# Kernel optimization log

Hardware: AMD Instinct MI355X
Metric: run time of the kernel (lower is better)

## Reference

```python
import jax, jax.numpy as jnp
import numpy as np


def setup_inputs() -> dict:
    key = jax.random.key(0)
    k1, k2 = jax.random.split(key)
    B, Tc, Tq, D = 8, 2048, 1024, 1024
    similarity = jax.random.normal(k1, (B, Tc, Tq), dtype=jnp.float32)
    qencode = jax.random.normal(k2, (B, Tq, D), dtype=jnp.float32)
    return {"similarity": similarity, "qencode": qencode}


def reference(similarity, qencode):
    # softmax over query axis, then weighted sum of query encodings:
    # equivalent to softmax(similarity, -1) @ qencode, avoiding the
    # [B, Tc, Tq, D] broadcasted intermediate of the original TF code.
    attn = jax.nn.softmax(similarity, axis=-1)          # [B, Tc, Tq]
    c2q = jnp.einsum("bcq,bqd->bcd", attn, qencode)     # [B, Tc, D]
    return c2q
```

## Files before the change

kernel.cpp:

```cpp
#include <hip/hip_runtime.h>
#include <hip/hip_bf16.h>
#include <stdint.h>

#define BATCH 8
#define TC 2048
#define TQ 1024
#define DD 1024

typedef __attribute__((ext_vector_type(8))) __bf16 bf16x8;
typedef __attribute__((ext_vector_type(4))) float f32x4;

__device__ __forceinline__ ushort f2bf(float f) {
    uint32_t u = __float_as_uint(f);
    uint32_t r = (u + 0x7fffu + ((u >> 16) & 1u)) >> 16;
    return (ushort)r;
}

__global__ __launch_bounds__(256) void prep(const float* __restrict__ sim,
                                            const float* __restrict__ qen,
                                            ushort* __restrict__ attn,
                                            ushort* __restrict__ qt) {
    __shared__ float tile[64][65];
    const int t = threadIdx.x;
    if (blockIdx.x < 4096) {
        const int wid = t >> 6;
        const int lane = t & 63;
        const int row = blockIdx.x * 4 + wid;
        const float4* src = (const float4*)(sim + (size_t)row * TQ);

        float4 x[4];
        #pragma unroll
        for (int j = 0; j < 4; j++) x[j] = src[lane + 64 * j];

        float m = -INFINITY;
        #pragma unroll
        for (int j = 0; j < 4; j++)
            m = fmaxf(m, fmaxf(fmaxf(x[j].x, x[j].y), fmaxf(x[j].z, x[j].w)));
        #pragma unroll
        for (int o = 32; o >= 1; o >>= 1) m = fmaxf(m, __shfl_xor(m, o));

        const float L2E = 1.4426950408889634f;
        float e[4][4];
        float s = 0.f;
        #pragma unroll
        for (int j = 0; j < 4; j++) {
            e[j][0] = exp2f((x[j].x - m) * L2E);
            e[j][1] = exp2f((x[j].y - m) * L2E);
            e[j][2] = exp2f((x[j].z - m) * L2E);
            e[j][3] = exp2f((x[j].w - m) * L2E);
            s += (e[j][0] + e[j][1]) + (e[j][2] + e[j][3]);
        }
        #pragma unroll
        for (int o = 32; o >= 1; o >>= 1) s += __shfl_xor(s, o);
        const float inv = 1.0f / s;

        ushort4* dst = (ushort4*)(attn + (size_t)row * TQ);
        #pragma unroll
        for (int j = 0; j < 4; j++) {
            ushort4 o4;
            o4.x = f2bf(e[j][0] * inv);
            o4.y = f2bf(e[j][1] * inv);
            o4.z = f2bf(e[j][2] * inv);
            o4.w = f2bf(e[j][3] * inv);
            dst[lane + 64 * j] = o4;
        }
    } else {
        const int bid = blockIdx.x - 4096;
        const int b = bid >> 8;
        const int rem = bid & 255;
        const int q0 = (rem >> 4) * 64;
        const int d0 = (rem & 15) * 64;
        const int r = t >> 4;
        const int c = (t & 15) * 4;

        #pragma unroll
        for (int it = 0; it < 4; it++) {
            float4 v = *(const float4*)(qen + ((size_t)b * TQ + q0 + r + it * 16) * DD + d0 + c);
            tile[r + it * 16][c + 0] = v.x;
            tile[r + it * 16][c + 1] = v.y;
            tile[r + it * 16][c + 2] = v.z;
            tile[r + it * 16][c + 3] = v.w;
        }
        __syncthreads();

        #pragma unroll
        for (int it = 0; it < 4; it++) {
            const int d = (t >> 4) + it * 16;
            const int qq = (t & 15) * 4;
            ushort4 o4;
            o4.x = f2bf(tile[qq + 0][d]);
            o4.y = f2bf(tile[qq + 1][d]);
            o4.z = f2bf(tile[qq + 2][d]);
            o4.w = f2bf(tile[qq + 3][d]);
            *(ushort4*)(qt + ((size_t)b * DD + d0 + d) * TQ + q0 + qq) = o4;
        }
    }
}

__global__ __launch_bounds__(256, 2) void gemm_bf16(const ushort* __restrict__ A,
                                                    const ushort* __restrict__ Bt,
                                                    float* __restrict__ C) {
    __shared__ __align__(16) ushort As[128 * 64];
    __shared__ __align__(16) ushort Bs[128 * 64];

    const int flat = blockIdx.x;
    const int b = flat >> 7;
    const int rem = flat & 127;
    const int group = rem >> 5;
    const int mi_t = group * 4 + (rem & 3);
    const int ni_t = (rem >> 2) & 7;
    const int tm0 = mi_t * 128;
    const int tn0 = ni_t * 128;

    const ushort* Ab = A + (size_t)b * TC * TQ;
    const ushort* Bb = Bt + (size_t)b * DD * TQ;
    float* Cb = C + (size_t)b * TC * DD;

    const int t = threadIdx.x;
    const int w = t >> 6, lane = t & 63;
    const int quad = lane >> 4, l16 = lane & 15;
    const int wm = (w >> 1) * 64, wn = (w & 1) * 64;

    f32x4 acc[4][4];
    #pragma unroll
    for (int i = 0; i < 4; i++)
        #pragma unroll
        for (int j = 0; j < 4; j++) acc[i][j] = (f32x4){0.f, 0.f, 0.f, 0.f};

    const int srow = w * 8 + (lane >> 3);
    const int sk = ((lane & 7) ^ (lane >> 3)) * 8;

    const int rkey = l16 & 7;

    for (int kk = 0; kk < TQ; kk += 64) {
        #pragma unroll
        for (int i = 0; i < 4; i++) {
            const ushort* ga = Ab + (size_t)(tm0 + i * 32 + srow) * TQ + kk + sk;
            const ushort* gb = Bb + (size_t)(tn0 + i * 32 + srow) * TQ + kk + sk;
            char* la = (char*)As + i * 4096 + w * 1024;
            char* lb = (char*)Bs + i * 4096 + w * 1024;
            __builtin_amdgcn_global_load_lds(
                (const __attribute__((address_space(1))) void*)ga,
                (__attribute__((address_space(3))) void*)la, 16, 0, 0);
            __builtin_amdgcn_global_load_lds(
                (const __attribute__((address_space(1))) void*)gb,
                (__attribute__((address_space(3))) void*)lb, 16, 0, 0);
        }
        __syncthreads();

        #pragma unroll
        for (int s = 0; s < 2; s++) {
            const int rswz = ((s * 4 + quad) ^ rkey) * 8;
            bf16x8 af[4], bfr[4];
            #pragma unroll
            for (int mi = 0; mi < 4; mi++)
                af[mi] = *(const bf16x8*)&As[(wm + mi * 16 + l16) * 64 + rswz];
            #pragma unroll
            for (int ni = 0; ni < 4; ni++)
                bfr[ni] = *(const bf16x8*)&Bs[(wn + ni * 16 + l16) * 64 + rswz];

            #pragma unroll
            for (int mi = 0; mi < 4; mi++)
                #pragma unroll
                for (int ni = 0; ni < 4; ni++)
                    acc[mi][ni] = __builtin_amdgcn_mfma_f32_16x16x32_bf16(
                        af[mi], bfr[ni], acc[mi][ni], 0, 0, 0);
        }
        __syncthreads();
    }

    #pragma unroll
    for (int mi = 0; mi < 4; mi++) {
        const int r0 = tm0 + wm + mi * 16 + quad * 4;
        #pragma unroll
        for (int ni = 0; ni < 4; ni++) {
            const int c = tn0 + wn + ni * 16 + l16;
            f32x4 v = acc[mi][ni];
            #pragma unroll
            for (int r = 0; r < 4; r++) Cb[(size_t)(r0 + r) * DD + c] = v[r];
        }
    }
}

extern "C" void kernel_launch(void* const* d_in, const int* in_sizes, int n_in,
                              void* d_out, int out_size, void* d_ws, size_t ws_size,
                              hipStream_t stream) {
    const float* sim = (const float*)d_in[0];
    const float* qen = (const float*)d_in[1];
    float* out = (float*)d_out;

    ushort* attn = (ushort*)d_ws;
    ushort* qt = (ushort*)d_ws + (size_t)BATCH * TC * TQ;

    prep<<<4096 + 2048, 256, 0, stream>>>(sim, qen, attn, qt);
    gemm_bf16<<<BATCH * (TC / 128) * (DD / 128), 256, 0, stream>>>(attn, qt, out);
}
```

Before: 178.2 us.

## Rewrite GEMM as 256x256 tile, 8-wave, double-buffered pipelined kernel

Replaces the 128x128 single-buffered GEMM with a 256x256 tile and 512 threads. LDS is double-buffered and global->LDS loads are interleaved with MFMA sub-phases using barriers, waitcnt and setprio to overlap memory with compute. A new block swizzle maps tiles to blocks. The larger tile raises arithmetic intensity but leaves only 256 blocks, which may underfill the GPU, and it uses 128KB of LDS and many accumulator registers.

```diff
diff --git a/kernel.cpp b/kernel.cpp
--- a/kernel.cpp
+++ b/kernel.cpp
@@ -97,87 +97,161 @@
     }
 }
 
-__global__ __launch_bounds__(256, 2) void gemm_bf16(const ushort* __restrict__ A,
+#define BAR()   __builtin_amdgcn_s_barrier()
+#define LGKM0() asm volatile("s_waitcnt lgkmcnt(0)" ::: "memory")
+#define PRIO(x) __builtin_amdgcn_s_setprio(x)
+
+#define KTILE(BUF, S1, S2, S3, S4, WEND)                                           \
+    {                                                                              \
+        bf16x8 aLO[4][2], aHI[4][2], bLO[2][2], bHI[2][2];                         \
+                         \
+        _Pragma("unroll") for (int mi = 0; mi < 4; ++mi)                           \
+            _Pragma("unroll") for (int ss = 0; ss < 2; ++ss)                       \
+                aLO[mi][ss] = *(const bf16x8*)&As[BUF][wm][mi * 16 + l16]          \
+                                  [((ss * 4 + quad) ^ rkey) * 8];                  \
+        _Pragma("unroll") for (int ni = 0; ni < 2; ++ni)                           \
+            _Pragma("unroll") for (int ss = 0; ss < 2; ++ss)                       \
+                bLO[ni][ss] = *(const bf16x8*)&Bs[BUF][wbh][wrow + ni * 16 + l16]  \
+                                  [((ss * 4 + quad) ^ rkey) * 8];                  \
+        S1;                                                                        \
+        BAR(); LGKM0(); PRIO(1);                                                   \
+        _Pragma("unroll") for (int mi = 0; mi < 4; ++mi)                           \
+            _Pragma("unroll") for (int ni = 0; ni < 2; ++ni)                       \
+                _Pragma("unroll") for (int ss = 0; ss < 2; ++ss)                   \
+                    acc[mi][ni] = __builtin_amdgcn_mfma_f32_16x16x32_bf16(         \
+                        aLO[mi][ss], bLO[ni][ss], acc[mi][ni], 0, 0, 0);           \
+        PRIO(0); BAR();                                                            \
+                                             \
+        _Pragma("unroll") for (int mi = 0; mi < 4; ++mi)                           \
+            _Pragma("unroll") for (int ss = 0; ss < 2; ++ss)                       \
+                aHI[mi][ss] = *(const bf16x8*)&As[BUF][wm][64 + mi * 16 + l16]     \
+                                  [((ss * 4 + quad) ^ rkey) * 8];                  \
+        S2;                                                                        \
+        BAR(); LGKM0(); PRIO(1);                                                   \
+        _Pragma("unroll") for (int mi = 0; mi < 4; ++mi)                           \
+            _Pragma("unroll") for (int ni = 0; ni < 2; ++ni)                       \
+                _Pragma("unroll") for (int ss = 0; ss < 2; ++ss)                   \
+                    acc[4 + mi][ni] = __builtin_amdgcn_mfma_f32_16x16x32_bf16(     \
+                        aHI[mi][ss], bLO[ni][ss], acc[4 + mi][ni], 0, 0, 0);       \
+        PRIO(0); BAR();                                                            \
+                                                    \
+        _Pragma("unroll") for (int ni = 0; ni < 2; ++ni)                           \
+            _Pragma("unroll") for (int ss = 0; ss < 2; ++ss)                       \
+                bHI[ni][ss] = *(const bf16x8*)&Bs[BUF][wbh]                        \
+                                  [wrow + 32 + ni * 16 + l16]                      \
+                                  [((ss * 4 + quad) ^ rkey) * 8];                  \
+        S3;                                                                        \
+        BAR(); LGKM0(); PRIO(1);                                                   \
+        _Pragma("unroll") for (int mi = 0; mi < 4; ++mi)                           \
+            _Pragma("unroll") for (int ni = 0; ni < 2; ++ni)                       \
+                _Pragma("unroll") for (int ss = 0; ss < 2; ++ss)                   \
+                    acc[mi][2 + ni] = __builtin_amdgcn_mfma_f32_16x16x32_bf16(     \
+                        aLO[mi][ss], bHI[ni][ss], acc[mi][2 + ni], 0, 0, 0);       \
+        PRIO(0); BAR();                                                            \
+                                                  \
+        S4;                                                                        \
+        BAR(); PRIO(1);                                                            \
+        _Pragma("unroll") for (int mi = 0; mi < 4; ++mi)                           \
+            _Pragma("unroll") for (int ni = 0; ni < 2; ++ni)                       \
+                _Pragma("unroll") for (int ss = 0; ss < 2; ++ss)                   \
+                    acc[4 + mi][2 + ni] = __builtin_amdgcn_mfma_f32_16x16x32_bf16( \
+                        aHI[mi][ss], bHI[ni][ss], acc[4 + mi][2 + ni], 0, 0, 0);   \
+        PRIO(0);                                                                   \
+        WEND;                                                                      \
+        BAR();                                                                     \
+    }
+
+__global__ __launch_bounds__(512, 2) void gemm_bf16(const ushort* __restrict__ A,
                                                     const ushort* __restrict__ Bt,
                                                     float* __restrict__ C) {
-    __shared__ __align__(16) ushort As[128 * 64];
-    __shared__ __align__(16) ushort Bs[128 * 64];
-
-    const int flat = blockIdx.x;
-    const int b = flat >> 7;
-    const int rem = flat & 127;
-    const int group = rem >> 5;
-    const int mi_t = group * 4 + (rem & 3);
-    const int ni_t = (rem >> 2) & 7;
-    const int tm0 = mi_t * 128;
-    const int tn0 = ni_t * 128;
+    __shared__ __align__(16) ushort As[2][2][128][64];
+    __shared__ __align__(16) ushort Bs[2][2][128][64];
+
+    const int bid = blockIdx.x;
+    const int swz = ((bid & 7) << 5) | (bid >> 3);
+    const int b   = swz >> 5;
+    const int tm0 = ((swz >> 2) & 7) * 256;
+    const int tn0 = (swz & 3) * 256;
 
     const ushort* Ab = A + (size_t)b * TC * TQ;
     const ushort* Bb = Bt + (size_t)b * DD * TQ;
     float* Cb = C + (size_t)b * TC * DD;
 
     const int t = threadIdx.x;
-    const int w = t >> 6, lane = t & 63;
+    const int wid = t >> 6, lane = t & 63;
     const int quad = lane >> 4, l16 = lane & 15;
-    const int wm = (w >> 1) * 64, wn = (w & 1) * 64;
-
-    f32x4 acc[4][4];
+    const int wm = wid >> 2;
+    const int wn = wid & 3;
+    const int wbh = wn >> 1;
+    const int wrow = (wn & 1) << 6;
+    const int rkey = l16 & 7;
+
+    const int srow = t >> 3;
+    const int gko  = (((t & 7) ^ (srow & 7)) << 3);
+
+    auto stageA = [&](int buf, int h, int kk) {
+        const ushort* g0 = Ab + (size_t)(tm0 + h * 128 + srow) * TQ + kk + gko;
+        char* l0 = (char*)(&As[buf][h][0][0]) + wid * 1024;
+        __builtin_amdgcn_global_load_lds(
+            (const __attribute__((address_space(1))) void*)g0,
+            (__attribute__((address_space(3))) void*)l0, 16, 0, 0);
+        __builtin_amdgcn_global_load_lds(
+            (const __attribute__((address_space(1))) void*)(g0 + (size_t)64 * TQ),
+            (__attribute__((address_space(3))) void*)(l0 + 8192), 16, 0, 0);
+    };
+    auto stageB = [&](int buf, int h, int kk) {
+        const ushort* g0 = Bb + (size_t)(tn0 + h * 128 + srow) * TQ + kk + gko;
+        char* l0 = (char*)(&Bs[buf][h][0][0]) + wid * 1024;
+        __builtin_amdgcn_global_load_lds(
+            (const __attribute__((address_space(1))) void*)g0,
+            (__attribute__((address_space(3))) void*)l0, 16, 0, 0);
+        __builtin_amdgcn_global_load_lds(
+            (const __attribute__((address_space(1))) void*)(g0 + (size_t)64 * TQ),
+            (__attribute__((address_space(3))) void*)(l0 + 8192), 16, 0, 0);
+    };
+
+    f32x4 acc[8][4];
     #pragma unroll
-    for (int i = 0; i < 4; i++)
+    for (int i = 0; i < 8; i++)
         #pragma unroll
         for (int j = 0; j < 4; j++) acc[i][j] = (f32x4){0.f, 0.f, 0.f, 0.f};
 
-    const int srow = w * 8 + (lane >> 3);
-    const int sk = ((lane & 7) ^ (lane >> 3)) * 8;
-
-    const int rkey = l16 & 7;
-
-    for (int kk = 0; kk < TQ; kk += 64) {
-        #pragma unroll
-        for (int i = 0; i < 4; i++) {
-            const ushort* ga = Ab + (size_t)(tm0 + i * 32 + srow) * TQ + kk + sk;
-            const ushort* gb = Bb + (size_t)(tn0 + i * 32 + srow) * TQ + kk + sk;
-            char* la = (char*)As + i * 4096 + w * 1024;
-            char* lb = (char*)Bs + i * 4096 + w * 1024;
-            __builtin_amdgcn_global_load_lds(
-                (const __attribute__((address_space(1))) void*)ga,
-                (__attribute__((address_space(3))) void*)la, 16, 0, 0);
-            __builtin_amdgcn_global_load_lds(
-                (const __attribute__((address_space(1))) void*)gb,
-                (__attribute__((address_space(3))) void*)lb, 16, 0, 0);
-        }
-        __syncthreads();
-
-        #pragma unroll
-        for (int s = 0; s < 2; s++) {
-            const int rswz = ((s * 4 + quad) ^ rkey) * 8;
-            bf16x8 af[4], bfr[4];
-            #pragma unroll
-            for (int mi = 0; mi < 4; mi++)
-                af[mi] = *(const bf16x8*)&As[(wm + mi * 16 + l16) * 64 + rswz];
-            #pragma unroll
-            for (int ni = 0; ni < 4; ni++)
-                bfr[ni] = *(const bf16x8*)&Bs[(wn + ni * 16 + l16) * 64 + rswz];
-
-            #pragma unroll
-            for (int mi = 0; mi < 4; mi++)
-                #pragma unroll
-                for (int ni = 0; ni < 4; ni++)
-                    acc[mi][ni] = __builtin_amdgcn_mfma_f32_16x16x32_bf16(
-                        af[mi], bfr[ni], acc[mi][ni], 0, 0, 0);
-        }
-        __syncthreads();
-    }
+    stageA(0, 0, 0);  stageA(0, 1, 0);  stageB(0, 0, 0);  stageB(0, 1, 0);
+    stageA(1, 0, 64); stageA(1, 1, 64); stageB(1, 0, 64); stageB(1, 1, 64);
+    asm volatile("s_waitcnt vmcnt(8)" ::: "memory");
+    BAR();
+
+    #pragma unroll 1
+    for (int it = 0; it < 7; ++it) {
+        const int kA = (2 * it + 2) * 64;
+        const int kB = (2 * it + 3) * 64;
+        KTILE(0,
+              (void)0,
+              (void)0,
+              stageA(0, 0, kA),
+              stageA(0, 1, kA),
+              asm volatile("s_waitcnt vmcnt(4)" ::: "memory"));
+        KTILE(1,
+              stageB(0, 0, kA),
+              stageB(0, 1, kA),
+              (stageA(1, 0, kB), stageA(1, 1, kB)),
+              (stageB(1, 0, kB), stageB(1, 1, kB)),
+              asm volatile("s_waitcnt vmcnt(8)" ::: "memory"));
+    }
+
+    KTILE(0, (void)0, (void)0, (void)0, (void)0,
+          asm volatile("s_waitcnt vmcnt(0)" ::: "memory"));
+    KTILE(1, (void)0, (void)0, (void)0, (void)0, (void)0);
 
     #pragma unroll
-    for (int mi = 0; mi < 4; mi++) {
-        const int r0 = tm0 + wm + mi * 16 + quad * 4;
-        #pragma unroll
-        for (int ni = 0; ni < 4; ni++) {
-            const int c = tn0 + wn + ni * 16 + l16;
+    for (int mi = 0; mi < 8; ++mi) {
+        const int r0 = tm0 + wm * 128 + mi * 16 + quad * 4;
+        #pragma unroll
+        for (int ni = 0; ni < 4; ++ni) {
+            const int c = tn0 + wn * 64 + ni * 16 + l16;
             f32x4 v = acc[mi][ni];
             #pragma unroll
-            for (int r = 0; r < 4; r++) Cb[(size_t)(r0 + r) * DD + c] = v[r];
+            for (int r = 0; r < 4; ++r) Cb[(size_t)(r0 + r) * DD + c] = v[r];
         }
     }
 }
@@ -193,5 +267,5 @@
     ushort* qt = (ushort*)d_ws + (size_t)BATCH * TC * TQ;
 
     prep<<<4096 + 2048, 256, 0, stream>>>(sim, qen, attn, qt);
-    gemm_bf16<<<BATCH * (TC / 128) * (DD / 128), 256, 0, stream>>>(attn, qt, out);
-}
+    gemm_bf16<<<BATCH * (TC / 256) * (DD / 256), 512, 0, stream>>>(attn, qt, out);
+}
```

After: 180.0 us. No clear change (+1.1%).

## Rewrite GEMM as 256x256 tile, 8-wave double-buffered pipeline with interleaved MFMA

Applied to the files above, without the earlier changes.

The bf16 GEMM now uses 256x256 output tiles with 512 threads per block and a double-buffered LDS ring. The next K-slice is prefetched with global_load_lds while the current one is consumed. LDS fragment reads are interleaved with MFMA groups under explicit lgkmcnt waits and s_setprio, and the block index is swizzled across batches. The goal is to hide global-load latency and raise arithmetic intensity per tile. In exchange it uses more LDS and registers (128 KB LDS per block and a larger accumulator array), and with 256 blocks on a GPU with many CUs occupancy may be limited.

```diff
diff --git a/kernel.cpp b/kernel.cpp
--- a/kernel.cpp
+++ b/kernel.cpp
@@ -97,87 +97,193 @@
     }
 }
 
-__global__ __launch_bounds__(256, 2) void gemm_bf16(const ushort* __restrict__ A,
+#define BAR()    __builtin_amdgcn_s_barrier()
+#define LGKM(n)  asm volatile("s_waitcnt lgkmcnt(" #n ")" ::: "memory")
+#define VMCNT0() asm volatile("s_waitcnt vmcnt(0)" ::: "memory")
+#define PRIO(x)  __builtin_amdgcn_s_setprio(x)
+
+__global__ __launch_bounds__(512, 2) void gemm_bf16(const ushort* __restrict__ A,
                                                     const ushort* __restrict__ Bt,
                                                     float* __restrict__ C) {
-    __shared__ __align__(16) ushort As[128 * 64];
-    __shared__ __align__(16) ushort Bs[128 * 64];
-
-    const int flat = blockIdx.x;
-    const int b = flat >> 7;
-    const int rem = flat & 127;
-    const int group = rem >> 5;
-    const int mi_t = group * 4 + (rem & 3);
-    const int ni_t = (rem >> 2) & 7;
-    const int tm0 = mi_t * 128;
-    const int tn0 = ni_t * 128;
+    __shared__ __align__(16) ushort As[2][2][128][64];
+    __shared__ __align__(16) ushort Bs[2][2][128][64];
+
+    const int bid = blockIdx.x;
+    const int swz = ((bid & 7) << 5) | (bid >> 3);
+    const int b   = swz >> 5;
+    const int tm0 = ((swz >> 2) & 7) * 256;
+    const int tn0 = (swz & 3) * 256;
 
     const ushort* Ab = A + (size_t)b * TC * TQ;
     const ushort* Bb = Bt + (size_t)b * DD * TQ;
     float* Cb = C + (size_t)b * TC * DD;
 
     const int t = threadIdx.x;
-    const int w = t >> 6, lane = t & 63;
+    const int wid = t >> 6, lane = t & 63;
     const int quad = lane >> 4, l16 = lane & 15;
-    const int wm = (w >> 1) * 64, wn = (w & 1) * 64;
-
-    f32x4 acc[4][4];
+    const int wm = wid >> 2;
+    const int wn = wid & 3;
+    const int wbh = wn >> 1;
+    const int wrow = (wn & 1) << 6;
+    const int rkey = l16 & 7;
+
+    const int srow = t >> 3;
+    const int gko  = (((t & 7) ^ (srow & 7)) << 3);
+
+    auto stageA = [&](int buf, int h, int kk) {
+        const ushort* g0 = Ab + (size_t)(tm0 + h * 128 + srow) * TQ + kk + gko;
+        char* l0 = (char*)(&As[buf][h][0][0]) + wid * 1024;
+        __builtin_amdgcn_global_load_lds(
+            (const __attribute__((address_space(1))) void*)g0,
+            (__attribute__((address_space(3))) void*)l0, 16, 0, 0);
+        __builtin_amdgcn_global_load_lds(
+            (const __attribute__((address_space(1))) void*)(g0 + (size_t)64 * TQ),
+            (__attribute__((address_space(3))) void*)(l0 + 8192), 16, 0, 0);
+    };
+    auto stageB = [&](int buf, int h, int kk) {
+        const ushort* g0 = Bb + (size_t)(tn0 + h * 128 + srow) * TQ + kk + gko;
+        char* l0 = (char*)(&Bs[buf][h][0][0]) + wid * 1024;
+        __builtin_amdgcn_global_load_lds(
+            (const __attribute__((address_space(1))) void*)g0,
+            (__attribute__((address_space(3))) void*)l0, 16, 0, 0);
+        __builtin_amdgcn_global_load_lds(
+            (const __attribute__((address_space(1))) void*)(g0 + (size_t)64 * TQ),
+            (__attribute__((address_space(3))) void*)(l0 + 8192), 16, 0, 0);
+    };
+
+    auto rdA = [&](int buf, int rb, int ss) -> bf16x8 {
+        return *(const bf16x8*)&As[buf][wm][rb * 16 + l16][((ss * 4 + quad) ^ rkey) * 8];
+    };
+    auto rdB = [&](int buf, int nb, int ss) -> bf16x8 {
+        return *(const bf16x8*)&Bs[buf][wbh][wrow + nb * 16 + l16][((ss * 4 + quad) ^ rkey) * 8];
+    };
+
+    f32x4 acc[8][4];
     #pragma unroll
-    for (int i = 0; i < 4; i++)
+    for (int i = 0; i < 8; i++)
         #pragma unroll
         for (int j = 0; j < 4; j++) acc[i][j] = (f32x4){0.f, 0.f, 0.f, 0.f};
 
-    const int srow = w * 8 + (lane >> 3);
-    const int sk = ((lane & 7) ^ (lane >> 3)) * 8;
-
-    const int rkey = l16 & 7;
-
-    for (int kk = 0; kk < TQ; kk += 64) {
-        #pragma unroll
-        for (int i = 0; i < 4; i++) {
-            const ushort* ga = Ab + (size_t)(tm0 + i * 32 + srow) * TQ + kk + sk;
-            const ushort* gb = Bb + (size_t)(tn0 + i * 32 + srow) * TQ + kk + sk;
-            char* la = (char*)As + i * 4096 + w * 1024;
-            char* lb = (char*)Bs + i * 4096 + w * 1024;
-            __builtin_amdgcn_global_load_lds(
-                (const __attribute__((address_space(1))) void*)ga,
-                (__attribute__((address_space(3))) void*)la, 16, 0, 0);
-            __builtin_amdgcn_global_load_lds(
-                (const __attribute__((address_space(1))) void*)gb,
-                (__attribute__((address_space(3))) void*)lb, 16, 0, 0);
-        }
-        __syncthreads();
-
-        #pragma unroll
-        for (int s = 0; s < 2; s++) {
-            const int rswz = ((s * 4 + quad) ^ rkey) * 8;
-            bf16x8 af[4], bfr[4];
-            #pragma unroll
-            for (int mi = 0; mi < 4; mi++)
-                af[mi] = *(const bf16x8*)&As[(wm + mi * 16 + l16) * 64 + rswz];
-            #pragma unroll
-            for (int ni = 0; ni < 4; ni++)
-                bfr[ni] = *(const bf16x8*)&Bs[(wn + ni * 16 + l16) * 64 + rswz];
-
-            #pragma unroll
-            for (int mi = 0; mi < 4; mi++)
-                #pragma unroll
-                for (int ni = 0; ni < 4; ni++)
-                    acc[mi][ni] = __builtin_amdgcn_mfma_f32_16x16x32_bf16(
-                        af[mi], bfr[ni], acc[mi][ni], 0, 0, 0);
-        }
-        __syncthreads();
+    stageA(0, 0, 0); stageA(0, 1, 0); stageB(0, 0, 0); stageB(0, 1, 0);
+    VMCNT0();
+
+    #pragma unroll 1
+    for (int x = 0; x < 16; ++x) {
+        const int bs = x & 1;
+        BAR();
+
+        bf16x8 aS0[4], aS1[4], bS0[2], bS1[2], c0[2], c1[2], d0[4], d1[4], e0[2], e1[2];
+
+        #pragma unroll
+        for (int i = 0; i < 4; i++) aS0[i] = rdA(bs, i, 0);
+        #pragma unroll
+        for (int i = 0; i < 2; i++) bS0[i] = rdB(bs, i, 0);
+
+        if (x < 15) {
+            const int kk = (x + 1) * 64;
+            stageA(bs ^ 1, 0, kk); stageA(bs ^ 1, 1, kk);
+            stageB(bs ^ 1, 0, kk); stageB(bs ^ 1, 1, kk);
+        }
+
+        #pragma unroll
+        for (int i = 0; i < 4; i++) aS1[i] = rdA(bs, i, 1);
+        #pragma unroll
+        for (int i = 0; i < 2; i++) bS1[i] = rdB(bs, i, 1);
+        LGKM(6); PRIO(1);
+        #pragma unroll
+        for (int mi = 0; mi < 4; mi++)
+            #pragma unroll
+            for (int ni = 0; ni < 2; ni++)
+                acc[mi][ni] = __builtin_amdgcn_mfma_f32_16x16x32_bf16(
+                    aS0[mi], bS0[ni], acc[mi][ni], 0, 0, 0);
+        PRIO(0);
+
+        #pragma unroll
+        for (int i = 0; i < 2; i++) c0[i] = rdB(bs, 2 + i, 0);
+        LGKM(2); PRIO(1);
+        #pragma unroll
+        for (int mi = 0; mi < 4; mi++)
+            #pragma unroll
+            for (int ni = 0; ni < 2; ni++)
+                acc[mi][ni] = __builtin_amdgcn_mfma_f32_16x16x32_bf16(
+                    aS1[mi], bS1[ni], acc[mi][ni], 0, 0, 0);
+        PRIO(0);
+
+        #pragma unroll
+        for (int i = 0; i < 2; i++) c1[i] = rdB(bs, 2 + i, 1);
+        LGKM(2); PRIO(1);
+        #pragma unroll
+        for (int mi = 0; mi < 4; mi++)
+            #pragma unroll
+            for (int ni = 0; ni < 2; ni++)
+                acc[mi][2 + ni] = __builtin_amdgcn_mfma_f32_16x16x32_bf16(
+                    aS0[mi], c0[ni], acc[mi][2 + ni], 0, 0, 0);
+        PRIO(0);
+
+        #pragma unroll
+        for (int i = 0; i < 4; i++) d0[i] = rdA(bs, 4 + i, 0);
+        LGKM(4); PRIO(1);
+        #pragma unroll
+        for (int mi = 0; mi < 4; mi++)
+            #pragma unroll
+            for (int ni = 0; ni < 2; ni++)
+                acc[mi][2 + ni] = __builtin_amdgcn_mfma_f32_16x16x32_bf16(
+                    aS1[mi], c1[ni], acc[mi][2 + ni], 0, 0, 0);
+        PRIO(0);
+
+        #pragma unroll
+        for (int i = 0; i < 4; i++) d1[i] = rdA(bs, 4 + i, 1);
+        LGKM(4); PRIO(1);
+        #pragma unroll
+        for (int mi = 0; mi < 4; mi++)
+            #pragma unroll
+            for (int ni = 0; ni < 2; ni++)
+                acc[4 + mi][2 + ni] = __builtin_amdgcn_mfma_f32_16x16x32_bf16(
+                    d0[mi], c0[ni], acc[4 + mi][2 + ni], 0, 0, 0);
+        PRIO(0);
+
+        #pragma unroll
+        for (int i = 0; i < 2; i++) e0[i] = rdB(bs, i, 0);
+        LGKM(2); PRIO(1);
+        #pragma unroll
+        for (int mi = 0; mi < 4; mi++)
+            #pragma unroll
+            for (int ni = 0; ni < 2; ni++)
+                acc[4 + mi][2 + ni] = __builtin_amdgcn_mfma_f32_16x16x32_bf16(
+                    d1[mi], c1[ni], acc[4 + mi][2 + ni], 0, 0, 0);
+        PRIO(0);
+
+        #pragma unroll
+        for (int i = 0; i < 2; i++) e1[i] = rdB(bs, i, 1);
+        LGKM(2); PRIO(1);
+        #pragma unroll
+        for (int mi = 0; mi < 4; mi++)
+            #pragma unroll
+            for (int ni = 0; ni < 2; ni++)
+                acc[4 + mi][ni] = __builtin_amdgcn_mfma_f32_16x16x32_bf16(
+                    d0[mi], e0[ni], acc[4 + mi][ni], 0, 0, 0);
+        PRIO(0);
+
+        LGKM(0); PRIO(1);
+        #pragma unroll
+        for (int mi = 0; mi < 4; mi++)
+            #pragma unroll
+            for (int ni = 0; ni < 2; ni++)
+                acc[4 + mi][ni] = __builtin_amdgcn_mfma_f32_16x16x32_bf16(
+                    d1[mi], e1[ni], acc[4 + mi][ni], 0, 0, 0);
+        PRIO(0);
+        if (x < 15) VMCNT0();
     }
 
     #pragma unroll
-    for (int mi = 0; mi < 4; mi++) {
-        const int r0 = tm0 + wm + mi * 16 + quad * 4;
-        #pragma unroll
-        for (int ni = 0; ni < 4; ni++) {
-            const int c = tn0 + wn + ni * 16 + l16;
+    for (int mi = 0; mi < 8; ++mi) {
+        const int r0 = tm0 + wm * 128 + mi * 16 + quad * 4;
+        #pragma unroll
+        for (int ni = 0; ni < 4; ++ni) {
+            const int c = tn0 + wn * 64 + ni * 16 + l16;
             f32x4 v = acc[mi][ni];
             #pragma unroll
-            for (int r = 0; r < 4; r++) Cb[(size_t)(r0 + r) * DD + c] = v[r];
+            for (int r = 0; r < 4; ++r) Cb[(size_t)(r0 + r) * DD + c] = v[r];
         }
     }
 }
@@ -193,5 +299,5 @@
     ushort* qt = (ushort*)d_ws + (size_t)BATCH * TC * TQ;
 
     prep<<<4096 + 2048, 256, 0, stream>>>(sim, qen, attn, qt);
-    gemm_bf16<<<BATCH * (TC / 128) * (DD / 128), 256, 0, stream>>>(attn, qt, out);
+    gemm_bf16<<<BATCH * (TC / 256) * (DD / 256), 512, 0, stream>>>(attn, qt, out);
 }
```

New measurement: 185.8 us. +4.3%, slower.

## Fuse softmax normalization into GEMM A-load using precomputed row stats

Applied to the files above, without the earlier changes.

Replaces materializing the bf16 attention matrix with a row-statistics pass (max and inverse sum), then recomputes exp and normalization on the fly while loading A tiles in the GEMM. This removes the write and re-read of the bf16 attention buffer. In exchange, the GEMM reads fp32 similarity (twice the bytes per tile), recomputes exps for every N-tile, and loses asynchronous direct-to-LDS loads for A. The transpose kernel is also widened to 128 columns with 8-element packed stores.

```diff
diff --git a/kernel.cpp b/kernel.cpp
--- a/kernel.cpp
+++ b/kernel.cpp
@@ -9,6 +9,7 @@
 
 typedef __attribute__((ext_vector_type(8))) __bf16 bf16x8;
 typedef __attribute__((ext_vector_type(4))) float f32x4;
+typedef __attribute__((ext_vector_type(8))) ushort ushort8v;
 
 __device__ __forceinline__ ushort f2bf(float f) {
     uint32_t u = __float_as_uint(f);
@@ -16,90 +17,104 @@
     return (ushort)r;
 }
 
-__global__ __launch_bounds__(256) void prep(const float* __restrict__ sim,
-                                            const float* __restrict__ qen,
-                                            ushort* __restrict__ attn,
-                                            ushort* __restrict__ qt) {
-    __shared__ float tile[64][65];
+__global__ __launch_bounds__(256) void rowstats(const float* __restrict__ sim,
+                                                float2* __restrict__ stats) {
     const int t = threadIdx.x;
-    if (blockIdx.x < 4096) {
-        const int wid = t >> 6;
-        const int lane = t & 63;
-        const int row = blockIdx.x * 4 + wid;
-        const float4* src = (const float4*)(sim + (size_t)row * TQ);
-
-        float4 x[4];
-        #pragma unroll
-        for (int j = 0; j < 4; j++) x[j] = src[lane + 64 * j];
-
-        float m = -INFINITY;
-        #pragma unroll
-        for (int j = 0; j < 4; j++)
-            m = fmaxf(m, fmaxf(fmaxf(x[j].x, x[j].y), fmaxf(x[j].z, x[j].w)));
-        #pragma unroll
-        for (int o = 32; o >= 1; o >>= 1) m = fmaxf(m, __shfl_xor(m, o));
-
-        const float L2E = 1.4426950408889634f;
-        float e[4][4];
-        float s = 0.f;
-        #pragma unroll
-        for (int j = 0; j < 4; j++) {
-            e[j][0] = exp2f((x[j].x - m) * L2E);
-            e[j][1] = exp2f((x[j].y - m) * L2E);
-            e[j][2] = exp2f((x[j].z - m) * L2E);
-            e[j][3] = exp2f((x[j].w - m) * L2E);
-            s += (e[j][0] + e[j][1]) + (e[j][2] + e[j][3]);
-        }
-        #pragma unroll
-        for (int o = 32; o >= 1; o >>= 1) s += __shfl_xor(s, o);
-        const float inv = 1.0f / s;
-
-        ushort4* dst = (ushort4*)(attn + (size_t)row * TQ);
-        #pragma unroll
-        for (int j = 0; j < 4; j++) {
-            ushort4 o4;
-            o4.x = f2bf(e[j][0] * inv);
-            o4.y = f2bf(e[j][1] * inv);
-            o4.z = f2bf(e[j][2] * inv);
-            o4.w = f2bf(e[j][3] * inv);
-            dst[lane + 64 * j] = o4;
-        }
-    } else {
-        const int bid = blockIdx.x - 4096;
-        const int b = bid >> 8;
-        const int rem = bid & 255;
-        const int q0 = (rem >> 4) * 64;
-        const int d0 = (rem & 15) * 64;
-        const int r = t >> 4;
-        const int c = (t & 15) * 4;
-
-        #pragma unroll
-        for (int it = 0; it < 4; it++) {
-            float4 v = *(const float4*)(qen + ((size_t)b * TQ + q0 + r + it * 16) * DD + d0 + c);
-            tile[r + it * 16][c + 0] = v.x;
-            tile[r + it * 16][c + 1] = v.y;
-            tile[r + it * 16][c + 2] = v.z;
-            tile[r + it * 16][c + 3] = v.w;
-        }
-        __syncthreads();
-
-        #pragma unroll
-        for (int it = 0; it < 4; it++) {
-            const int d = (t >> 4) + it * 16;
-            const int qq = (t & 15) * 4;
-            ushort4 o4;
-            o4.x = f2bf(tile[qq + 0][d]);
-            o4.y = f2bf(tile[qq + 1][d]);
-            o4.z = f2bf(tile[qq + 2][d]);
-            o4.w = f2bf(tile[qq + 3][d]);
-            *(ushort4*)(qt + ((size_t)b * DD + d0 + d) * TQ + q0 + qq) = o4;
-        }
-    }
-}
-
-__global__ __launch_bounds__(256, 2) void gemm_bf16(const ushort* __restrict__ A,
-                                                    const ushort* __restrict__ Bt,
-                                                    float* __restrict__ C) {
+    const int wid = t >> 6, lane = t & 63;
+    const int r0 = blockIdx.x * 8 + wid * 2;
+
+    const float4* s0 = (const float4*)(sim + (size_t)r0 * TQ);
+    const float4* s1 = (const float4*)(sim + (size_t)(r0 + 1) * TQ);
+
+    float4 x0[4], x1[4];
+    #pragma unroll
+    for (int j = 0; j < 4; j++) { x0[j] = s0[lane + 64 * j]; x1[j] = s1[lane + 64 * j]; }
+
+    float m0 = -INFINITY, m1 = -INFINITY;
+    #pragma unroll
+    for (int j = 0; j < 4; j++) {
+        m0 = fmaxf(m0, fmaxf(fmaxf(x0[j].x, x0[j].y), fmaxf(x0[j].z, x0[j].w)));
+        m1 = fmaxf(m1, fmaxf(fmaxf(x1[j].x, x1[j].y), fmaxf(x1[j].z, x1[j].w)));
+    }
+    #pragma unroll
+    for (int o = 32; o >= 1; o >>= 1) {
+        m0 = fmaxf(m0, __shfl_xor(m0, o));
+        m1 = fmaxf(m1, __shfl_xor(m1, o));
+    }
+
+    const float L2E = 1.4426950408889634f;
+    float sa = 0.f, sb = 0.f;
+    #pragma unroll
+    for (int j = 0; j < 4; j++) {
+        {
+            float e0 = exp2f((x0[j].x - m0) * L2E);
+            float e1 = exp2f((x0[j].y - m0) * L2E);
+            float e2 = exp2f((x0[j].z - m0) * L2E);
+            float e3 = exp2f((x0[j].w - m0) * L2E);
+            sa += (e0 + e1) + (e2 + e3);
+        }
+        {
+            float e0 = exp2f((x1[j].x - m1) * L2E);
+            float e1 = exp2f((x1[j].y - m1) * L2E);
+            float e2 = exp2f((x1[j].z - m1) * L2E);
+            float e3 = exp2f((x1[j].w - m1) * L2E);
+            sb += (e0 + e1) + (e2 + e3);
+        }
+    }
+    #pragma unroll
+    for (int o = 32; o >= 1; o >>= 1) {
+        sa += __shfl_xor(sa, o);
+        sb += __shfl_xor(sb, o);
+    }
+
+    if (lane == 0) {
+        float4 out = make_float4(m0, 1.0f / sa, m1, 1.0f / sb);
+        *(float4*)&stats[r0] = out;
+    }
+}
+
+__global__ __launch_bounds__(256) void transp(const float* __restrict__ qen,
+                                              ushort* __restrict__ qt) {
+    __shared__ float tile[64][133];
+    const int t = threadIdx.x;
+    const int bid = blockIdx.x;
+    const int b = bid >> 7;
+    const int rem = bid & 127;
+    const int q0 = (rem >> 3) * 64;
+    const int d0 = (rem & 7) * 128;
+
+    const int r0 = t >> 5;
+    const int cf = (t & 31) * 4;
+
+    float4 v[8];
+    #pragma unroll
+    for (int it = 0; it < 8; it++)
+        v[it] = *(const float4*)(qen + ((size_t)b * TQ + q0 + r0 + it * 8) * DD + d0 + cf);
+    #pragma unroll
+    for (int it = 0; it < 8; it++) {
+        tile[r0 + it * 8][cf + 0] = v[it].x;
+        tile[r0 + it * 8][cf + 1] = v[it].y;
+        tile[r0 + it * 8][cf + 2] = v[it].z;
+        tile[r0 + it * 8][cf + 3] = v[it].w;
+    }
+    __syncthreads();
+
+    const int q8 = (t & 7) * 8;
+    const int dbase = t >> 3;
+    #pragma unroll
+    for (int j2 = 0; j2 < 4; j2++) {
+        const int d = dbase + 32 * j2;
+        ushort8v pk;
+        #pragma unroll
+        for (int j = 0; j < 8; j++) pk[j] = f2bf(tile[q8 + j][d]);
+        *(ushort8v*)(qt + ((size_t)b * DD + d0 + d) * TQ + q0 + q8) = pk;
+    }
+}
+
+__global__ __launch_bounds__(256, 2) void gemm_fused(const float* __restrict__ S,
+                                                     const float2* __restrict__ st,
+                                                     const ushort* __restrict__ Bt,
+                                                     float* __restrict__ C) {
     __shared__ __align__(16) ushort As[128 * 64];
     __shared__ __align__(16) ushort Bs[128 * 64];
 
@@ -112,7 +127,7 @@
     const int tm0 = mi_t * 128;
     const int tn0 = ni_t * 128;
 
-    const ushort* Ab = A + (size_t)b * TC * TQ;
+    const float* Sb = S + (size_t)b * TC * TQ;
     const ushort* Bb = Bt + (size_t)b * DD * TQ;
     float* Cb = C + (size_t)b * TC * DD;
 
@@ -129,22 +144,44 @@
 
     const int srow = w * 8 + (lane >> 3);
     const int sk = ((lane & 7) ^ (lane >> 3)) * 8;
-
     const int rkey = l16 & 7;
 
+    const float L2E = 1.4426950408889634f;
+
+    float2 stv[4];
+    #pragma unroll
+    for (int i = 0; i < 4; i++)
+        stv[i] = st[(size_t)b * TC + tm0 + i * 32 + srow];
+
     for (int kk = 0; kk < TQ; kk += 64) {
+        float4 xa[4][2];
         #pragma unroll
         for (int i = 0; i < 4; i++) {
-            const ushort* ga = Ab + (size_t)(tm0 + i * 32 + srow) * TQ + kk + sk;
+            const float* g = Sb + (size_t)(tm0 + i * 32 + srow) * TQ + kk + sk;
+            xa[i][0] = *(const float4*)g;
+            xa[i][1] = *(const float4*)(g + 4);
+        }
+        #pragma unroll
+        for (int i = 0; i < 4; i++) {
             const ushort* gb = Bb + (size_t)(tn0 + i * 32 + srow) * TQ + kk + sk;
-            char* la = (char*)As + i * 4096 + w * 1024;
             char* lb = (char*)Bs + i * 4096 + w * 1024;
-            __builtin_amdgcn_global_load_lds(
-                (const __attribute__((address_space(1))) void*)ga,
-                (__attribute__((address_space(3))) void*)la, 16, 0, 0);
             __builtin_amdgcn_global_load_lds(
                 (const __attribute__((address_space(1))) void*)gb,
                 (__attribute__((address_space(3))) void*)lb, 16, 0, 0);
+        }
+        #pragma unroll
+        for (int i = 0; i < 4; i++) {
+            const float mm = stv[i].x, iv = stv[i].y;
+            ushort8v pk;
+            pk[0] = f2bf(exp2f((xa[i][0].x - mm) * L2E) * iv);
+            pk[1] = f2bf(exp2f((xa[i][0].y - mm) * L2E) * iv);
+            pk[2] = f2bf(exp2f((xa[i][0].z - mm) * L2E) * iv);
+            pk[3] = f2bf(exp2f((xa[i][0].w - mm) * L2E) * iv);
+            pk[4] = f2bf(exp2f((xa[i][1].x - mm) * L2E) * iv);
+            pk[5] = f2bf(exp2f((xa[i][1].y - mm) * L2E) * iv);
+            pk[6] = f2bf(exp2f((xa[i][1].z - mm) * L2E) * iv);
+            pk[7] = f2bf(exp2f((xa[i][1].w - mm) * L2E) * iv);
+            *(ushort8v*)&As[i * 2048 + w * 512 + lane * 8] = pk;
         }
         __syncthreads();
 
@@ -189,9 +226,10 @@
     const float* qen = (const float*)d_in[1];
     float* out = (float*)d_out;
 
-    ushort* attn = (ushort*)d_ws;
-    ushort* qt = (ushort*)d_ws + (size_t)BATCH * TC * TQ;
-
-    prep<<<4096 + 2048, 256, 0, stream>>>(sim, qen, attn, qt);
-    gemm_bf16<<<BATCH * (TC / 128) * (DD / 128), 256, 0, stream>>>(attn, qt, out);
-}
+    ushort* qt = (ushort*)d_ws;
+    float2* stats = (float2*)((char*)d_ws + (size_t)BATCH * DD * TQ * 2);
+
+    rowstats<<<BATCH * TC / 8, 256, 0, stream>>>(sim, stats);
+    transp<<<BATCH * (TQ / 64) * (DD / 128), 256, 0, stream>>>(qen, qt);
+    gemm_fused<<<BATCH * (TC / 128) * (DD / 128), 256, 0, stream>>>(sim, stats, qt, out);
+}
```

Measured after the change: 211.1 us. 18.5% more time.
